# Performance work log

Measured on AMD Instinct MI355X. Metric: run time of the kernel, lower is better.

## Reference

```python
import jax, jax.numpy as jnp
import numpy as np

B, N, CIN, COUT, NS, S = 16, 512, 512, 512, 16, 8
EPS = 1e-5


def _bn(y, g, b):
    # eval-mode BatchNorm1d: running_mean=0, running_var=1 (fresh module buffers)
    return y * (g / jnp.sqrt(1.0 + EPS)) + b


def setup_inputs():
    key = jax.random.key(0)
    ks = jax.random.split(key, 16)

    def lin(k, fi, fo):
        kw, kb = jax.random.split(k)
        s = 1.0 / np.sqrt(fi)
        return (jax.random.uniform(kw, (fi, fo), minval=-s, maxval=s),
                jax.random.uniform(kb, (fo,), minval=-s, maxval=s))

    Wq, bq = lin(ks[0], CIN, COUT)
    Wk, bk = lin(ks[1], CIN, COUT)
    Wv, bv = lin(ks[2], CIN, COUT)
    p1_W, p1_b = lin(ks[3], 3, 3)
    p2_W, p2_b = lin(ks[4], 3, COUT)
    w1_W, w1_b = lin(ks[5], COUT, COUT // S)
    w2_W, w2_b = lin(ks[6], COUT // S, COUT // S)
    return dict(
        p=jax.random.uniform(ks[7], (B, N, 3)),
        x=jax.random.normal(ks[8], (B, CIN, N)),
        Wq=Wq, bq=bq, Wk=Wk, bk=bk, Wv=Wv, bv=bv,
        p1_W=p1_W, p1_b=p1_b,
        p_bn_g=1.0 + 0.1 * jax.random.normal(ks[9], (3,)),
        p_bn_b=0.1 * jax.random.normal(ks[10], (3,)),
        p2_W=p2_W, p2_b=p2_b,
        w_bn1_g=1.0 + 0.1 * jax.random.normal(ks[11], (COUT,)),
        w_bn1_b=0.1 * jax.random.normal(ks[12], (COUT,)),
        w1_W=w1_W, w1_b=w1_b,
        w_bn2_g=1.0 + 0.1 * jax.random.normal(ks[13], (COUT // S,)),
        w_bn2_b=0.1 * jax.random.normal(ks[14], (COUT // S,)),
        w2_W=w2_W, w2_b=w2_b,
    )


def reference(p, x, Wq, bq, Wk, bk, Wv, bv, p1_W, p1_b, p_bn_g, p_bn_b,
              p2_W, p2_b, w_bn1_g, w_bn1_b, w1_W, w1_b, w_bn2_g, w_bn2_b,
              w2_W, w2_b):
    xt = x.transpose(0, 2, 1)                     # (B,N,CIN)
    xq = xt @ Wq + bq                             # (B,N,COUT)
    xk = xt @ Wk + bk
    xv = xt @ Wv + bv
    # kNN over points (self-query): squared distances, then 16 smallest
    sq = jnp.sum(p * p, axis=-1)                  # (B,N)
    d = sq[:, :, None] + sq[:, None, :] - 2.0 * jnp.einsum('bnd,bmd->bnm', p, p)
    _, idx = jax.lax.top_k(-d, NS)                # (B,N,NS), includes self
    gather = jax.vmap(lambda f, i: f[i])          # per-batch fancy gather
    k_g = gather(xk, idx)                         # (B,N,NS,COUT)
    v_g = gather(xv, idx)                         # (B,N,NS,COUT)
    p_r = gather(p, idx) - p[:, :, None, :]       # relative coords (B,N,NS,3)
    # linear_p: Linear(3,3) -> BN(3) -> ReLU -> Linear(3,COUT)
    pr = jax.nn.relu(_bn(p_r @ p1_W + p1_b, p_bn_g, p_bn_b)) @ p2_W + p2_b
    # vector attention logits; out_planes//mid_planes == 1 so the .sum(3) is identity
    w = k_g - xq[:, :, None, :] + pr              # (B,N,NS,COUT)
    # linear_w: BN -> ReLU -> Linear(C, C//s) -> BN -> ReLU -> Linear(C//s, C//s)
    w = jax.nn.relu(_bn(w, w_bn1_g, w_bn1_b)) @ w1_W + w1_b
    w = jax.nn.relu(_bn(w, w_bn2_g, w_bn2_b)) @ w2_W + w2_b
    w = jax.nn.softmax(w, axis=2)                 # softmax over neighbors
    out = ((v_g + pr).reshape(B, N, NS, S, COUT // S)
           * w[:, :, :, None, :]).sum(2)          # (B,N,S,COUT//S)
    return out.reshape(B, N, COUT)
```

## Files before the change

### kernel.cpp

```cpp
#include <hip/hip_runtime.h>

typedef unsigned short u16;
typedef unsigned int   u32;

#define Bv  16
#define Nv  512
#define Cv  512
#define NSv 16
#define CCv 64

typedef __attribute__((ext_vector_type(8))) short bf16x8;
typedef __attribute__((ext_vector_type(4))) float f32x4;

__device__ __forceinline__ u16 f2bf(float f) {
  u32 b = __float_as_uint(f);
  return (u16)((b + 0x7fffu + ((b >> 16) & 1u)) >> 16);
}
__device__ __forceinline__ u32 pack2(float lo, float hi) {
  return (u32)f2bf(lo) | ((u32)f2bf(hi) << 16);
}
__device__ __forceinline__ u32 cvtpk(float lo, float hi) {
  u32 r;
  asm("v_cvt_pk_bf16_f32 %0, %1, %2" : "=v"(r) : "v"(lo), "v"(hi));
  return r;
}
__device__ __forceinline__ float bfl(u32 w) { return __uint_as_float(w << 16); }
__device__ __forceinline__ float bfh(u32 w) { return __uint_as_float(w & 0xffff0000u); }

__global__ __launch_bounds__(256) void prep_kernel(
    const float* __restrict__ p, int* __restrict__ idx_out,
    const float* __restrict__ x,
    const float* __restrict__ Wq, const float* __restrict__ Wk, const float* __restrict__ Wv,
    const float* __restrict__ w1W, const float* __restrict__ w2W,
    u16* __restrict__ xbT, u16* __restrict__ Wcat,
    u16* __restrict__ w1p, u16* __restrict__ w2p) {
  __shared__ __align__(16) char ARB[16640];
  const int t = threadIdx.x;
  if (blockIdx.x < 256) {
#pragma clang fp contract(off)
    float4* pnts = (float4*)ARB;
    const int b  = blockIdx.x >> 4;
    const int q0 = (blockIdx.x & 15) * 32;
    for (int e = t; e < Nv; e += 256) {
      float xx = p[(b * Nv + e) * 3 + 0];
      float yy = p[(b * Nv + e) * 3 + 1];
      float zz = p[(b * Nv + e) * 3 + 2];
      float s = ((xx * xx) + (yy * yy)) + (zz * zz);
      pnts[e] = make_float4(xx, yy, zz, s);
    }
    __syncthreads();
    const int q  = q0 + (t >> 3);
    const int pt = t & 7;
    const float4 qp = pnts[q];
    float bd[NSv]; int bi[NSv];
#pragma unroll
    for (int i = 0; i < NSv; i++) { bd[i] = 1e30f; bi[i] = 0; }
    const int m0 = pt * 64;
#pragma unroll 1
    for (int i = 0; i < 64; i++) {
      const int m = m0 + i;
      const float4 c = pnts[m];
      float dot = __builtin_fmaf(qp.z, c.z, __builtin_fmaf(qp.y, c.y, qp.x * c.x));
      float d = (qp.w + c.w) - (2.0f * dot);
      bool cm[NSv];
#pragma unroll
      for (int j = 0; j < NSv; j++) cm[j] = bd[j] > d;
#pragma unroll
      for (int j = NSv - 1; j > 0; j--) {
        bd[j] = cm[j - 1] ? bd[j - 1] : (cm[j] ? d : bd[j]);
        bi[j] = cm[j - 1] ? bi[j - 1] : (cm[j] ? m : bi[j]);
      }
      bd[0] = cm[0] ? d : bd[0];
      bi[0] = cm[0] ? m : bi[0];
    }
    int h = 0;
#pragma unroll 1
    for (int s = 0; s < 16; s++) {
      float mv = bd[0]; int ml = pt;
      {
        float ov = __shfl_xor(mv, 1); int ol = __shfl_xor(ml, 1);
        bool tk = (ov < mv) || (ov == mv && ol < ml);
        mv = tk ? ov : mv; ml = tk ? ol : ml;
      }
      {
        float ov = __shfl_xor(mv, 2); int ol = __shfl_xor(ml, 2);
        bool tk = (ov < mv) || (ov == mv && ol < ml);
        mv = tk ? ov : mv; ml = tk ? ol : ml;
      }
      {
        float ov = __shfl_xor(mv, 4); int ol = __shfl_xor(ml, 4);
        bool tk = (ov < mv) || (ov == mv && ol < ml);
        mv = tk ? ov : mv; ml = tk ? ol : ml;
      }
      if (ml == pt) {
#pragma unroll
        for (int j = 0; j < 15; j++) bd[j] = bd[j + 1];
        bd[15] = 1e30f;
        h++;
      }
    }
    const int lane = t & 63, gbase = lane & 56;
    int pre = 0;
#pragma unroll
    for (int j = 0; j < 7; j++) {
      int hj = __shfl(h, gbase + j);
      if (j < pt) pre += hj;
    }
    int* o = idx_out + (b * Nv + q) * NSv + pre;
#pragma unroll
    for (int j = 0; j < 16; j++)
      if (j < h) o[j] = bi[j];
  } else {
    float (*lt)[65] = (float(*)[65])ARB;
    const int id = blockIdx.x - 256;
    const int tile = id & 63, unit = id >> 6;
    const float* src; u16* dst;
    int k0, c0, srcC, dstC;
    if (unit < 16) {
      src = x + unit * 262144; dst = xbT + unit * 262144;
      k0 = (tile & 7) * 64; c0 = (tile >> 3) * 64; srcC = 512; dstC = 512;
    } else if (unit < 19) {
      const int mat = unit - 16;
      src = (mat == 0) ? Wq : (mat == 1) ? Wk : Wv;
      dst = Wcat + mat * 262144;
      k0 = (tile & 7) * 64; c0 = (tile >> 3) * 64; srcC = 512; dstC = 512;
    } else {
      if (tile < 8)       { src = w1W; dst = w1p; k0 = tile * 64; c0 = 0; srcC = 64; dstC = 512; }
      else if (tile == 8) { src = w2W; dst = w2p; k0 = 0; c0 = 0; srcC = 64; dstC = 64; }
      else return;
    }
    {
      const int r = t >> 2, cq = (t & 3) * 16;
      const float* s = src + (k0 + r) * srcC + c0 + cq;
#pragma unroll
      for (int i = 0; i < 4; i++) {
        const float4 v = *(const float4*)&s[i * 4];
        lt[r][cq + i * 4 + 0] = v.x;
        lt[r][cq + i * 4 + 1] = v.y;
        lt[r][cq + i * 4 + 2] = v.z;
        lt[r][cq + i * 4 + 3] = v.w;
      }
    }
    __syncthreads();
    {
      const int rr = t >> 2, kq = (t & 3) * 16;
      uint4 pa, pb;
      pa.x = pack2(lt[kq + 0][rr],  lt[kq + 1][rr]);
      pa.y = pack2(lt[kq + 2][rr],  lt[kq + 3][rr]);
      pa.z = pack2(lt[kq + 4][rr],  lt[kq + 5][rr]);
      pa.w = pack2(lt[kq + 6][rr],  lt[kq + 7][rr]);
      pb.x = pack2(lt[kq + 8][rr],  lt[kq + 9][rr]);
      pb.y = pack2(lt[kq + 10][rr], lt[kq + 11][rr]);
      pb.z = pack2(lt[kq + 12][rr], lt[kq + 13][rr]);
      pb.w = pack2(lt[kq + 14][rr], lt[kq + 15][rr]);
      u16* o = dst + (c0 + rr) * dstC + k0 + kq;
      *(uint4*)&o[0] = pa;
      *(uint4*)&o[8] = pb;
    }
  }
}

__global__ __launch_bounds__(256, 1) void qkv_mfma(
    const u16* __restrict__ xbT, const u16* __restrict__ Wcat,
    const float* __restrict__ bq, const float* __restrict__ bk, const float* __restrict__ bv,
    const float* __restrict__ bn1g, const float* __restrict__ bn1b, const float* __restrict__ p2b,
    u16* __restrict__ xqh, u16* __restrict__ xkh, float* __restrict__ xv) {
  __shared__ u32 Sh[320 * 16];
  const float rno = 1.0f / sqrtf(1.0f + 1e-5f);
  const int mt  = blockIdx.x;
  const int b   = mt >> 2;
  const int m0c = (mt & 3) * 128;
  const int j0  = blockIdx.y * 64;
  const int t   = threadIdx.x;
  const int lane = t & 63, w = t >> 6;
  const int l15 = lane & 15, quad = lane >> 4;

  const u16* asrc[2]; int adst[2];
#pragma unroll
  for (int rd = 0; rd < 2; rd++) {
    const int gidx = rd * 256 + t;
    const int r = gidx >> 2, g = gidx & 3, gd = g ^ (r & 3);
    asrc[rd] = xbT + (b * 512 + m0c + r) * 512 + gd * 8;
    adst[rd] = r * 16 + g * 4;
  }
  const u16* wsrc[3]; int wdst[3];
#pragma unroll
  for (int rd = 0; rd < 3; rd++) {
    const int gidx = rd * 256 + t;
    const int r = gidx >> 2, g = gidx & 3, gd = g ^ (r & 3);
    wsrc[rd] = Wcat + (r >> 6) * 262144 + (j0 + (r & 63)) * 512 + gd * 8;
    wdst[rd] = 2048 + r * 16 + g * 4;
  }

  f32x4 acc[4][3][2];
#pragma unroll
  for (int a1 = 0; a1 < 4; a1++)
#pragma unroll
    for (int a2 = 0; a2 < 3; a2++)
#pragma unroll
      for (int a3 = 0; a3 < 2; a3++) acc[a1][a2][a3] = (f32x4){0.f, 0.f, 0.f, 0.f};

  const int sa  = (quad ^ (l15 & 3)) * 4;
  const int ra0 = ((2 * w + 0) * 16 + l15) * 16;
  const int ra1 = ((2 * w + 1) * 16 + l15) * 16;

  auto mfma_step = [&]() {
    const bf16x8 a0 = *(const bf16x8*)&Sh[ra0 + sa];
    const bf16x8 a1 = *(const bf16x8*)&Sh[ra1 + sa];
#pragma unroll
    for (int js = 0; js < 4; js++)
#pragma unroll
      for (int mat = 0; mat < 3; mat++) {
        const bf16x8 bfr = *(const bf16x8*)&Sh[2048 + (mat * 64 + js * 16 + l15) * 16 + sa];
        acc[js][mat][0] = __builtin_amdgcn_mfma_f32_16x16x32_bf16(a0, bfr, acc[js][mat][0], 0, 0, 0);
        acc[js][mat][1] = __builtin_amdgcn_mfma_f32_16x16x32_bf16(a1, bfr, acc[js][mat][1], 0, 0, 0);
      }
  };

  uint4 rA[2], rW[3], sA[2], sW[3];
#pragma unroll
  for (int rd = 0; rd < 2; rd++) rA[rd] = *(const uint4*)&asrc[rd][0];
#pragma unroll
  for (int rd = 0; rd < 3; rd++) rW[rd] = *(const uint4*)&wsrc[rd][0];

  for (int k0 = 0; k0 < 512; k0 += 64) {
#pragma unroll
    for (int rd = 0; rd < 2; rd++) *(uint4*)&Sh[adst[rd]] = rA[rd];
#pragma unroll
    for (int rd = 0; rd < 3; rd++) *(uint4*)&Sh[wdst[rd]] = rW[rd];
#pragma unroll
    for (int rd = 0; rd < 2; rd++) sA[rd] = *(const uint4*)&asrc[rd][k0 + 32];
#pragma unroll
    for (int rd = 0; rd < 3; rd++) sW[rd] = *(const uint4*)&wsrc[rd][k0 + 32];
    __syncthreads();
    mfma_step();
    __syncthreads();
#pragma unroll
    for (int rd = 0; rd < 2; rd++) *(uint4*)&Sh[adst[rd]] = sA[rd];
#pragma unroll
    for (int rd = 0; rd < 3; rd++) *(uint4*)&Sh[wdst[rd]] = sW[rd];
    if (k0 + 64 < 512) {
#pragma unroll
      for (int rd = 0; rd < 2; rd++) rA[rd] = *(const uint4*)&asrc[rd][k0 + 64];
#pragma unroll
      for (int rd = 0; rd < 3; rd++) rW[rd] = *(const uint4*)&wsrc[rd][k0 + 64];
    }
    __syncthreads();
    mfma_step();
    __syncthreads();
  }

  float bias[4][3], s1v[4], Tv[4];
#pragma unroll
  for (int js = 0; js < 4; js++) {
    const int col = j0 + js * 16 + l15;
    bias[js][0] = bq[col];
    bias[js][1] = bk[col];
    bias[js][2] = bv[col];
    s1v[js] = bn1g[col] * rno;
    Tv[js]  = fmaf(p2b[col], s1v[js], bn1b[col]);
  }
#pragma unroll
  for (int js = 0; js < 4; js++)
#pragma unroll
    for (int mat = 0; mat < 3; mat++) {
      const int col = j0 + js * 16 + l15;
#pragma unroll
      for (int st = 0; st < 2; st++) {
        const int rbase = b * 512 + m0c + (2 * w + st) * 16 + quad * 4;
        const f32x4 v = acc[js][mat][st];
        if (mat == 2) {
#pragma unroll
          for (int reg = 0; reg < 4; reg++)
            xv[(rbase + reg) * 512 + col] = v[reg] + bias[js][2];
        } else if (mat == 0) {
#pragma unroll
          for (int reg = 0; reg < 4; reg++)
            xqh[(rbase + reg) * 512 + col] = f2bf((v[reg] + bias[js][0]) * s1v[js] - Tv[js]);
        } else {
#pragma unroll
          for (int reg = 0; reg < 4; reg++)
            xkh[(rbase + reg) * 512 + col] = f2bf((v[reg] + bias[js][1]) * s1v[js]);
        }
      }
    }
}

#define NQ  8
#define LSd 66

__global__ __launch_bounds__(256, 3) void attn_kernel(
    const float* __restrict__ p, const int* __restrict__ idx,
    const u16* __restrict__ xqh, const u16* __restrict__ xkh, const float* __restrict__ xv,
    const float* __restrict__ p1W, const float* __restrict__ p1b,
    const float* __restrict__ pbg, const float* __restrict__ pbb,
    const float* __restrict__ p2W, const float* __restrict__ p2b,
    const float* __restrict__ bn1g, const float* __restrict__ bn1b,
    const u16* __restrict__ w1p, const float* __restrict__ w1b,
    const float* __restrict__ bn2g, const float* __restrict__ bn2b,
    const u16* __restrict__ w2p, const float* __restrict__ w2b,
    float* __restrict__ out) {
  const float rno = 1.0f / sqrtf(1.0f + 1e-5f);
  const int s_  = blockIdx.x;
  const int xcd = s_ & 7, kk_ = s_ >> 3;
  const int b   = (xcd << 1) | (kk_ & 1);
  const int n0  = (kk_ >> 1) * NQ;
  const int t  = threadIdx.x;
  __shared__ float ARN[8448];
  __shared__ float h_s[128][3];
  __shared__ int   idx_s[128];
  float* A0f = ARN;
  float* A1f = ARN + 512;
  float* A2f = ARN + 1024;
  u32* wbf = (u32*)(ARN + 1536);
  u32* ubf = (u32*)(ARN + 3584);

  if (t < 128) idx_s[t] = idx[(b * Nv + n0 + (t >> 4)) * NSv + (t & 15)] & (Nv - 1);

  {
    const int c0 = t * 2;
#pragma unroll
    for (int i = 0; i < 2; i++) {
      const int c = c0 + i;
      const float s1 = bn1g[c] * rno;
      A0f[c] = p2W[c] * s1;
      A1f[c] = p2W[512 + c] * s1;
      A2f[c] = p2W[1024 + c] * s1;
    }
  }
  __syncthreads();

  for (int e = t; e < 384; e += 256) {
    const int row = e / 3, j = e % 3;
    const int m = idx_s[row];
    const int n = n0 + (row >> 4);
    float d0 = p[(b * Nv + m) * 3 + 0] - p[(b * Nv + n) * 3 + 0];
    float d1 = p[(b * Nv + m) * 3 + 1] - p[(b * Nv + n) * 3 + 1];
    float d2 = p[(b * Nv + m) * 3 + 2] - p[(b * Nv + n) * 3 + 2];
    float y = d0 * p1W[0 * 3 + j] + d1 * p1W[1 * 3 + j] + d2 * p1W[2 * 3 + j] + p1b[j];
    y = y * (pbg[j] * rno) + pbb[j];
    h_s[row][j] = fmaxf(y, 0.0f);
  }

  const int row = t >> 1, ci = (t & 1) * 32;
  const int mrow = idx_s[row];
  const u16* xkr = xkh + (b * Nv + mrow) * Cv + ci;
  const u16* xqr = xqh + (b * Nv + n0 + (row >> 4)) * Cv + ci;
  uint4 pf[4], pfq[4];
#pragma unroll
  for (int i = 0; i < 4; i++) {
    pf[i]  = *(const uint4*)&xkr[i * 8];
    pfq[i] = *(const uint4*)&xqr[i * 8];
  }
  __syncthreads();

  const int lane = t & 63, w = t >> 6;
  const int l15 = lane & 15, quad = lane >> 4;
  const float h0 = h_s[row][0], h1 = h_s[row][1], h2 = h_s[row][2];
  const int rsw = row & 7, half4 = (t & 1) * 4;

  int wrow[2], wg[2], wgd[2];
#pragma unroll
  for (int rd = 0; rd < 2; rd++) {
    const int gidx = rd * 256 + t;
    wrow[rd] = gidx >> 3; wg[rd] = gidx & 7; wgd[rd] = wg[rd] ^ (wrow[rd] & 7);
  }

  f32x4 acc[2][4];
#pragma unroll
  for (int a1 = 0; a1 < 2; a1++)
#pragma unroll
    for (int a2 = 0; a2 < 4; a2++) acc[a1][a2] = (f32x4){0.f, 0.f, 0.f, 0.f};

  for (int kc = 0; kc < Cv; kc += 64) {
    uint4 wr[2];
#pragma unroll
    for (int rd = 0; rd < 2; rd++)
      wr[rd] = *(const uint4*)&w1p[wrow[rd] * 512 + kc + wgd[rd] * 8];
    {
      u32* ub = &ubf[row * 32];
#pragma unroll
      for (int gi = 0; gi < 4; gi++) {
        const int c4 = kc + ci + gi * 8;
        const float4 A0a = *(const float4*)&A0f[c4], A0b = *(const float4*)&A0f[c4 + 4];
        const float4 A1a = *(const float4*)&A1f[c4], A1b = *(const float4*)&A1f[c4 + 4];
        const float4 A2a = *(const float4*)&A2f[c4], A2b = *(const float4*)&A2f[c4 + 4];
        const uint4 kw = pf[gi], qw = pfq[gi];
        const float d0 = bfl(kw.x) - bfl(qw.x);
        const float d1 = bfh(kw.x) - bfh(qw.x);
        const float d2 = bfl(kw.y) - bfl(qw.y);
        const float d3 = bfh(kw.y) - bfh(qw.y);
        const float d4 = bfl(kw.z) - bfl(qw.z);
        const float d5 = bfh(kw.z) - bfh(qw.z);
        const float d6 = bfl(kw.w) - bfl(qw.w);
        const float d7 = bfh(kw.w) - bfh(qw.w);
        const float u0 = fmaxf(fmaf(h0, A0a.x, fmaf(h1, A1a.x, fmaf(h2, A2a.x, d0))), 0.f);
        const float u1 = fmaxf(fmaf(h0, A0a.y, fmaf(h1, A1a.y, fmaf(h2, A2a.y, d1))), 0.f);
        const float u2 = fmaxf(fmaf(h0, A0a.z, fmaf(h1, A1a.z, fmaf(h2, A2a.z, d2))), 0.f);
        const float u3 = fmaxf(fmaf(h0, A0a.w, fmaf(h1, A1a.w, fmaf(h2, A2a.w, d3))), 0.f);
        const float u4 = fmaxf(fmaf(h0, A0b.x, fmaf(h1, A1b.x, fmaf(h2, A2b.x, d4))), 0.f);
        const float u5 = fmaxf(fmaf(h0, A0b.y, fmaf(h1, A1b.y, fmaf(h2, A2b.y, d5))), 0.f);
        const float u6 = fmaxf(fmaf(h0, A0b.z, fmaf(h1, A1b.z, fmaf(h2, A2b.z, d6))), 0.f);
        const float u7 = fmaxf(fmaf(h0, A0b.w, fmaf(h1, A1b.w, fmaf(h2, A2b.w, d7))), 0.f);
        uint4 pk;
        pk.x = cvtpk(u0, u1); pk.y = cvtpk(u2, u3);
        pk.z = cvtpk(u4, u5); pk.w = cvtpk(u6, u7);
        *(uint4*)&ub[((half4 + gi) ^ rsw) * 4] = pk;
      }
    }
    if (kc + 64 < Cv) {
#pragma unroll
      for (int i = 0; i < 4; i++) {
        pf[i]  = *(const uint4*)&xkr[kc + 64 + i * 8];
        pfq[i] = *(const uint4*)&xqr[kc + 64 + i * 8];
      }
    }
#pragma unroll
    for (int rd = 0; rd < 2; rd++)
      *(uint4*)&wbf[wrow[rd] * 32 + wg[rd] * 4] = wr[rd];
    __syncthreads();
#pragma unroll
    for (int ks = 0; ks < 2; ks++) {
      const int sw = ((ks * 4 + quad) ^ (l15 & 7)) * 4;
      const bf16x8 a0 = *(const bf16x8*)&ubf[((2 * w + 0) * 16 + l15) * 32 + sw];
      const bf16x8 a1 = *(const bf16x8*)&ubf[((2 * w + 1) * 16 + l15) * 32 + sw];
#pragma unroll
      for (int js = 0; js < 4; js++) {
        const bf16x8 bfr = *(const bf16x8*)&wbf[(js * 16 + l15) * 32 + sw];
        acc[0][js] = __builtin_amdgcn_mfma_f32_16x16x32_bf16(a0, bfr, acc[0][js], 0, 0, 0);
        acc[1][js] = __builtin_amdgcn_mfma_f32_16x16x32_bf16(a1, bfr, acc[1][js], 0, 0, 0);
      }
    }
    __syncthreads();
  }

  {
    u16* r1h = (u16*)ubf;
#pragma unroll
    for (int js = 0; js < 4; js++) {
      const int j = js * 16 + l15;
      const float wb = w1b[j], s2 = bn2g[j] * rno, b2 = bn2b[j];
      const int gph = j >> 3;
#pragma unroll
      for (int st = 0; st < 2; st++) {
        const int rbase = (2 * w + st) * 16 + quad * 4;
#pragma unroll
        for (int reg = 0; reg < 4; reg++) {
          const int r = rbase + reg;
          const float v = fmaxf((acc[st][js][reg] + wb) * s2 + b2, 0.f);
          r1h[r * 64 + (gph ^ (r & 7)) * 8 + (j & 7)] = f2bf(v);
        }
      }
    }
  }
#pragma unroll
  for (int rd = 0; rd < 2; rd++) {
    const uint4 v = *(const uint4*)&w2p[wrow[rd] * 64 + wgd[rd] * 8];
    *(uint4*)&wbf[wrow[rd] * 32 + wg[rd] * 4] = v;
  }
  __syncthreads();

  f32x4 acc2[2][4];
#pragma unroll
  for (int a1 = 0; a1 < 2; a1++)
#pragma unroll
    for (int a2 = 0; a2 < 4; a2++) acc2[a1][a2] = (f32x4){0.f, 0.f, 0.f, 0.f};
#pragma unroll
  for (int ks = 0; ks < 2; ks++) {
    const int sw = ((ks * 4 + quad) ^ (l15 & 7)) * 4;
    const bf16x8 a0 = *(const bf16x8*)&ubf[((2 * w + 0) * 16 + l15) * 32 + sw];
    const bf16x8 a1 = *(const bf16x8*)&ubf[((2 * w + 1) * 16 + l15) * 32 + sw];
#pragma unroll
    for (int js = 0; js < 4; js++) {
      const bf16x8 bfr = *(const bf16x8*)&wbf[(js * 16 + l15) * 32 + sw];
      acc2[0][js] = __builtin_amdgcn_mfma_f32_16x16x32_bf16(a0, bfr, acc2[0][js], 0, 0, 0);
      acc2[1][js] = __builtin_amdgcn_mfma_f32_16x16x32_bf16(a1, bfr, acc2[1][js], 0, 0, 0);
    }
  }
  __syncthreads();

  {
    float* lg = ARN;
#pragma unroll
    for (int js = 0; js < 4; js++) {
      const float wb2 = w2b[js * 16 + l15];
#pragma unroll
      for (int st = 0; st < 2; st++) {
        const int rbase = (2 * w + st) * 16 + quad * 4;
#pragma unroll
        for (int reg = 0; reg < 4; reg++)
          lg[(rbase + reg) * LSd + js * 16 + l15] = acc2[st][js][reg] + wb2;
      }
    }
  }
  __syncthreads();

#pragma unroll
  for (int pp = 0; pp < 2; pp++) {
    const int pair = t + pp * 256;
    const int q = pair >> 6, jj = pair & 63;
    float* base = &ARN[(q * 16) * LSd + jj];
    float v[NSv];
#pragma unroll
    for (int k = 0; k < NSv; k++) v[k] = base[k * LSd];
    float mx = v[0];
#pragma unroll
    for (int k = 1; k < NSv; k++) mx = fmaxf(mx, v[k]);
    float s = 0.0f;
#pragma unroll
    for (int k = 0; k < NSv; k++) { v[k] = expf(v[k] - mx); s += v[k]; }
    const float is = 1.0f / s;
#pragma unroll
    for (int k = 0; k < NSv; k++) base[k * LSd] = v[k] * is;
  }
  __syncthreads();

  {
    const int q = t >> 5, cb = t & 31;
    float hk0[NSv], hk1[NSv], hk2[NSv];
    int mk[NSv];
#pragma unroll
    for (int k = 0; k < NSv; k++) {
      hk0[k] = h_s[q * 16 + k][0];
      hk1[k] = h_s[q * 16 + k][1];
      hk2[k] = h_s[q * 16 + k][2];
      mk[k]  = idx_s[q * 16 + k];
    }
    const float* smb = &ARN[(q * 16) * LSd];
    float* ob = out + (b * Nv + n0 + q) * Cv;
#pragma unroll 1
    for (int i = 0; i < 16; i++) {
      const int c = cb + i * 32;
      const float pa = p2W[c], pb2 = p2W[512 + c], pc = p2W[1024 + c], pd = p2b[c];
      const int jj = c & 63;
      float s0 = 0.f, s1 = 0.f, s2 = 0.f, s3 = 0.f;
#pragma unroll
      for (int k = 0; k < NSv; k += 4) {
        const float pr0 = hk0[k + 0] * pa + hk1[k + 0] * pb2 + hk2[k + 0] * pc + pd;
        const float pr1 = hk0[k + 1] * pa + hk1[k + 1] * pb2 + hk2[k + 1] * pc + pd;
        const float pr2 = hk0[k + 2] * pa + hk1[k + 2] * pb2 + hk2[k + 2] * pc + pd;
        const float pr3 = hk0[k + 3] * pa + hk1[k + 3] * pb2 + hk2[k + 3] * pc + pd;
        s0 = fmaf(xv[(b * Nv + mk[k + 0]) * Cv + c] + pr0, smb[(k + 0) * LSd + jj], s0);
        s1 = fmaf(xv[(b * Nv + mk[k + 1]) * Cv + c] + pr1, smb[(k + 1) * LSd + jj], s1);
        s2 = fmaf(xv[(b * Nv + mk[k + 2]) * Cv + c] + pr2, smb[(k + 2) * LSd + jj], s2);
        s3 = fmaf(xv[(b * Nv + mk[k + 3]) * Cv + c] + pr3, smb[(k + 3) * LSd + jj], s3);
      }
      ob[c] = (s0 + s1) + (s2 + s3);
    }
  }
}

extern "C" void kernel_launch(void* const* d_in, const int* in_sizes, int n_in,
                              void* d_out, int out_size, void* d_ws, size_t ws_size,
                              hipStream_t stream) {
  const float* p    = (const float*)d_in[0];
  const float* x    = (const float*)d_in[1];
  const float* Wq   = (const float*)d_in[2];
  const float* bq   = (const float*)d_in[3];
  const float* Wk   = (const float*)d_in[4];
  const float* bk   = (const float*)d_in[5];
  const float* Wv   = (const float*)d_in[6];
  const float* bv   = (const float*)d_in[7];
  const float* p1W  = (const float*)d_in[8];
  const float* p1b  = (const float*)d_in[9];
  const float* pbg  = (const float*)d_in[10];
  const float* pbb  = (const float*)d_in[11];
  const float* p2W  = (const float*)d_in[12];
  const float* p2b  = (const float*)d_in[13];
  const float* bn1g = (const float*)d_in[14];
  const float* bn1b = (const float*)d_in[15];
  const float* w1W  = (const float*)d_in[16];
  const float* w1b  = (const float*)d_in[17];
  const float* bn2g = (const float*)d_in[18];
  const float* bn2b = (const float*)d_in[19];
  const float* w2W  = (const float*)d_in[20];
  const float* w2b  = (const float*)d_in[21];

  int*   idxb = (int*)d_ws;
  float* xv   = (float*)((char*)d_ws + 524288);
  u16*   xqh  = (u16*)(xv + 8192 * 512);
  u16*   xkh  = xqh + 8192 * 512;
  u16*   xbT  = xkh + 8192 * 512;
  u16*   Wcat = xbT + 8192 * 512;
  u16*   w1p  = Wcat + 3 * 512 * 512;
  u16*   w2p  = w1p + 64 * 512;

  prep_kernel<<<dim3(1536), 256, 0, stream>>>(p, idxb, x, Wq, Wk, Wv, w1W, w2W,
                                              xbT, Wcat, w1p, w2p);
  qkv_mfma<<<dim3(64, 8), 256, 0, stream>>>(xbT, Wcat, bq, bk, bv, bn1g, bn1b, p2b,
                                            xqh, xkh, xv);
  attn_kernel<<<dim3(1024), 256, 0, stream>>>(p, idxb, xqh, xkh, xv,
                                              p1W, p1b, pbg, pbb, p2W, p2b,
                                              bn1g, bn1b, w1p, w1b, bn2g, bn2b,
                                              w2p, w2b, (float*)d_out);
}
```

Measured before the change: 268.4 us.

## Double-buffer QKV GEMM LDS tiles using direct global-to-LDS loads

Replaces the register-staged LDS fill in the QKV MFMA GEMM with global_load_lds direct copies into a double-buffered shared tile. The next K slice now loads while the current one is multiplied, and there is one barrier per step instead of two. The LDS swizzle gains an extra XOR term to reduce bank conflicts under the new write pattern, and the min-blocks launch bound is removed. It also cuts register pressure, but LDS usage doubles and the wait on vmcnt(0) still serializes each step.

Result: faster. 231.9 us (-13.6%).

```diff
diff --git a/kernel.cpp b/kernel.cpp
--- a/kernel.cpp
+++ b/kernel.cpp
@@ -26,6 +26,11 @@
 }
 __device__ __forceinline__ float bfl(u32 w) { return __uint_as_float(w << 16); }
 __device__ __forceinline__ float bfh(u32 w) { return __uint_as_float(w & 0xffff0000u); }
+
+#define GLD_LDS16(gp, lp)                                                              \
+  __builtin_amdgcn_global_load_lds(                                                    \
+      (const __attribute__((address_space(1))) u32*)(const void*)(gp),                 \
+      (__attribute__((address_space(3))) u32*)(lp), 16, 0, 0)
 
 __global__ __launch_bounds__(256) void prep_kernel(
     const float* __restrict__ p, int* __restrict__ idx_out,
@@ -160,12 +165,12 @@
   }
 }
 
-__global__ __launch_bounds__(256, 1) void qkv_mfma(
+__global__ __launch_bounds__(256) void qkv_mfma(
     const u16* __restrict__ xbT, const u16* __restrict__ Wcat,
     const float* __restrict__ bq, const float* __restrict__ bk, const float* __restrict__ bv,
     const float* __restrict__ bn1g, const float* __restrict__ bn1b, const float* __restrict__ p2b,
     u16* __restrict__ xqh, u16* __restrict__ xkh, float* __restrict__ xv) {
-  __shared__ u32 Sh[320 * 16];
+  __shared__ u32 Sh[2][5120];
   const float rno = 1.0f / sqrtf(1.0f + 1e-5f);
   const int mt  = blockIdx.x;
   const int b   = mt >> 2;
@@ -175,21 +180,21 @@
   const int lane = t & 63, w = t >> 6;
   const int l15 = lane & 15, quad = lane >> 4;
 
-  const u16* asrc[2]; int adst[2];
+  const u16* asrc[2];
 #pragma unroll
   for (int rd = 0; rd < 2; rd++) {
     const int gidx = rd * 256 + t;
-    const int r = gidx >> 2, g = gidx & 3, gd = g ^ (r & 3);
+    const int r = gidx >> 2, g = gidx & 3;
+    const int gd = g ^ (r & 3) ^ ((r >> 2) & 3);
     asrc[rd] = xbT + (b * 512 + m0c + r) * 512 + gd * 8;
-    adst[rd] = r * 16 + g * 4;
-  }
-  const u16* wsrc[3]; int wdst[3];
+  }
+  const u16* wsrc[3];
 #pragma unroll
   for (int rd = 0; rd < 3; rd++) {
     const int gidx = rd * 256 + t;
-    const int r = gidx >> 2, g = gidx & 3, gd = g ^ (r & 3);
+    const int r = gidx >> 2, g = gidx & 3;
+    const int gd = g ^ (r & 3) ^ ((r >> 2) & 3);
     wsrc[rd] = Wcat + (r >> 6) * 262144 + (j0 + (r & 63)) * 512 + gd * 8;
-    wdst[rd] = 2048 + r * 16 + g * 4;
   }
 
   f32x4 acc[4][3][2];
@@ -200,54 +205,42 @@
 #pragma unroll
       for (int a3 = 0; a3 < 2; a3++) acc[a1][a2][a3] = (f32x4){0.f, 0.f, 0.f, 0.f};
 
-  const int sa  = (quad ^ (l15 & 3)) * 4;
+  const int sa  = (quad ^ (l15 & 3) ^ ((l15 >> 2) & 3)) * 4;
   const int ra0 = ((2 * w + 0) * 16 + l15) * 16;
   const int ra1 = ((2 * w + 1) * 16 + l15) * 16;
 
-  auto mfma_step = [&]() {
-    const bf16x8 a0 = *(const bf16x8*)&Sh[ra0 + sa];
-    const bf16x8 a1 = *(const bf16x8*)&Sh[ra1 + sa];
+  auto stage = [&](int buf, int k0) {
+#pragma unroll
+    for (int rd = 0; rd < 2; rd++)
+      GLD_LDS16(asrc[rd] + k0, &Sh[buf][(rd * 256 + w * 64) * 4]);
+#pragma unroll
+    for (int rd = 0; rd < 3; rd++)
+      GLD_LDS16(wsrc[rd] + k0, &Sh[buf][2048 + (rd * 256 + w * 64) * 4]);
+  };
+  auto mfma_step = [&](int buf) {
+    const u32* S = Sh[buf];
+    const bf16x8 a0 = *(const bf16x8*)&S[ra0 + sa];
+    const bf16x8 a1 = *(const bf16x8*)&S[ra1 + sa];
 #pragma unroll
     for (int js = 0; js < 4; js++)
 #pragma unroll
       for (int mat = 0; mat < 3; mat++) {
-        const bf16x8 bfr = *(const bf16x8*)&Sh[2048 + (mat * 64 + js * 16 + l15) * 16 + sa];
+        const bf16x8 bfr = *(const bf16x8*)&S[2048 + (mat * 64 + js * 16 + l15) * 16 + sa];
         acc[js][mat][0] = __builtin_amdgcn_mfma_f32_16x16x32_bf16(a0, bfr, acc[js][mat][0], 0, 0, 0);
         acc[js][mat][1] = __builtin_amdgcn_mfma_f32_16x16x32_bf16(a1, bfr, acc[js][mat][1], 0, 0, 0);
       }
   };
 
-  uint4 rA[2], rW[3], sA[2], sW[3];
-#pragma unroll
-  for (int rd = 0; rd < 2; rd++) rA[rd] = *(const uint4*)&asrc[rd][0];
-#pragma unroll
-  for (int rd = 0; rd < 3; rd++) rW[rd] = *(const uint4*)&wsrc[rd][0];
-
-  for (int k0 = 0; k0 < 512; k0 += 64) {
-#pragma unroll
-    for (int rd = 0; rd < 2; rd++) *(uint4*)&Sh[adst[rd]] = rA[rd];
-#pragma unroll
-    for (int rd = 0; rd < 3; rd++) *(uint4*)&Sh[wdst[rd]] = rW[rd];
-#pragma unroll
-    for (int rd = 0; rd < 2; rd++) sA[rd] = *(const uint4*)&asrc[rd][k0 + 32];
-#pragma unroll
-    for (int rd = 0; rd < 3; rd++) sW[rd] = *(const uint4*)&wsrc[rd][k0 + 32];
+  stage(0, 0);
+  asm volatile("s_waitcnt vmcnt(0)" ::: "memory");
+  __syncthreads();
+  int cur = 0;
+  for (int k0 = 0; k0 < 512; k0 += 32) {
+    if (k0 + 32 < 512) stage(cur ^ 1, k0 + 32);
+    mfma_step(cur);
+    asm volatile("s_waitcnt vmcnt(0)" ::: "memory");
     __syncthreads();
-    mfma_step();
-    __syncthreads();
-#pragma unroll
-    for (int rd = 0; rd < 2; rd++) *(uint4*)&Sh[adst[rd]] = sA[rd];
-#pragma unroll
-    for (int rd = 0; rd < 3; rd++) *(uint4*)&Sh[wdst[rd]] = sW[rd];
-    if (k0 + 64 < 512) {
-#pragma unroll
-      for (int rd = 0; rd < 2; rd++) rA[rd] = *(const uint4*)&asrc[rd][k0 + 64];
-#pragma unroll
-      for (int rd = 0; rd < 3; rd++) rW[rd] = *(const uint4*)&wsrc[rd][k0 + 64];
-    }
-    __syncthreads();
-    mfma_step();
-    __syncthreads();
+    cur ^= 1;
   }
 
   float bias[4][3], s1v[4], Tv[4];
```
